# Performance work log

Hardware: AMD Instinct MI355X
Metric: run time of the kernel (lower is better)

Reference implementation:

```python
import jax, jax.numpy as jnp
import numpy as np
import math

B, T, C = 4, 2048, 1024
NH, D = 16, 64  # n_head, head_dim; NH * D == C


def setup_inputs() -> dict:
    key = jax.random.key(0)
    ks = jax.random.split(key, 7)
    std = 0.02
    return {
        "x": jax.random.normal(ks[0], (B, T, C), dtype=jnp.float32),
        "W_attn": jax.random.normal(ks[1], (C, 3 * C), dtype=jnp.float32) * std,
        "b_attn": jax.random.normal(ks[2], (3 * C,), dtype=jnp.float32) * std,
        "bQ": jax.random.normal(ks[3], (NH, D), dtype=jnp.float32) * 0.1 + 0.5,
        "bK": jax.random.normal(ks[4], (NH, D), dtype=jnp.float32) * 0.1 + 0.3,
        "W_proj": jax.random.normal(ks[5], (C, C), dtype=jnp.float32) * std,
        "b_proj": jax.random.normal(ks[6], (C,), dtype=jnp.float32) * std,
    }


def reference(x, W_attn, b_attn, bQ, bK, W_proj, b_proj):
    Bx, Tx, Cx = x.shape
    qkv = x @ W_attn + b_attn                      # [B, T, 3C]
    q, k, v = jnp.split(qkv, 3, axis=2)
    # [B, T, C] -> [B, NH, T, D]
    q = q.reshape(Bx, Tx, NH, D).transpose(0, 2, 1, 3)
    k = k.reshape(Bx, Tx, NH, D).transpose(0, 2, 1, 3)
    v = v.reshape(Bx, Tx, NH, D).transpose(0, 2, 1, 3)
    # per-head disorder bias added to Q and K before the dot product
    q = q + bQ[None, :, None, :]
    k = k + bK[None, :, None, :]
    scores = jnp.einsum('bhqd,bhkd->bhqk', q, k) / math.sqrt(D)  # [B, NH, T, T]
    causal = jnp.tril(jnp.ones((Tx, Tx), dtype=bool))
    scores = jnp.where(causal[None, None], scores, jnp.float32(-jnp.inf))
    att = jax.nn.softmax(scores, axis=-1)
    y = jnp.einsum('bhqk,bhkd->bhqd', att, v)      # [B, NH, T, D]
    y = y.transpose(0, 2, 1, 3).reshape(Bx, Tx, Cx)
    return y @ W_proj + b_proj
```

## Files before the change

### kernel.cpp

```cpp
#include <hip/hip_runtime.h>

typedef unsigned short u16;
typedef unsigned int u32;
typedef unsigned long long u64;
typedef __bf16 bf16x8 __attribute__((ext_vector_type(8)));
typedef float f32x4 __attribute__((ext_vector_type(4)));

#define B_  4
#define T_  2048
#define C_  1024
#define NH_ 16
#define D_  64
#define M_  (B_*T_)
#define N_QKV (3*C_)

#define ATTN_BLOCKS 1024

#define BARRIER()  __asm__ __volatile__("s_barrier" ::: "memory")
#define WAIT_VM4() __asm__ __volatile__("s_waitcnt vmcnt(4)" ::: "memory")
#define WAIT_VM8() __asm__ __volatile__("s_waitcnt vmcnt(8)" ::: "memory")
#define WAIT_VM0() __asm__ __volatile__("s_waitcnt vmcnt(0)" ::: "memory")
#define LGKM0()    __asm__ __volatile__("s_waitcnt lgkmcnt(0)" ::: "memory")

__device__ __forceinline__ void async_copy16(void* lds, const void* gptr) {
  __builtin_amdgcn_global_load_lds(
      (const __attribute__((address_space(1))) u32*)gptr,
      (__attribute__((address_space(3))) u32*)(u32)(uintptr_t)lds,
      16, 0, 0);
}

__device__ __forceinline__ u16 f2bf(float f) {
  union { float f; unsigned u; } c; c.f = f;
  unsigned u = c.u;
  unsigned r = (u + 0x7fffu + ((u >> 16) & 1u)) >> 16;
  return (u16)r;
}

__global__ __launch_bounds__(256) void conv_bf16(const float* __restrict__ in,
                                                 u16* __restrict__ out, int n) {
  int i = (blockIdx.x * 256 + threadIdx.x) * 4;
  if (i < n) {
    float4 f = *reinterpret_cast<const float4*>(in + i);
    u16 o[4] = { f2bf(f.x), f2bf(f.y), f2bf(f.z), f2bf(f.w) };
    *reinterpret_cast<uint2*>(out + i) = *reinterpret_cast<uint2*>(o);
  }
}

__global__ __launch_bounds__(256) void transpose_bf16(const float* __restrict__ in,
                                                      u16* __restrict__ out,
                                                      int K, int N) {
  __shared__ float tile[32][33];
  int bi = blockIdx.y;
  int bj = blockIdx.x;
  int tx = threadIdx.x & 31;
  int ty = threadIdx.x >> 5;
#pragma unroll
  for (int i = 0; i < 4; ++i) {
    int row = ty + i * 8;
    tile[row][tx] = in[(bi * 32 + row) * N + bj * 32 + tx];
  }
  __syncthreads();
#pragma unroll
  for (int i = 0; i < 4; ++i) {
    int row = ty + i * 8;
    out[(bj * 32 + row) * K + bi * 32 + tx] = f2bf(tile[tx][row]);
  }
}

__global__ __launch_bounds__(256, 2) void gemm_qkv(const u16* __restrict__ A,
                                                   const u16* __restrict__ Bt,
                                                   const float* __restrict__ b_attn,
                                                   const float* __restrict__ bQ,
                                                   const float* __restrict__ bK,
                                                   u16* __restrict__ qo,
                                                   u16* __restrict__ ko,
                                                   u16* __restrict__ vo) {
  const int K = C_;
  int bid = blockIdx.x;
  int wg = (bid & 7) * 192 + (bid >> 3);
  int bm = wg / 24, bn = wg % 24;
  const bool qk = (bn < 16);

  int tid = threadIdx.x;
  int wid = tid >> 6, lane = tid & 63;
  int lm = lane & 15, lq = lane >> 4;
  int wm = (wid >> 1) * 64, wn = (wid & 1) * 64;

  __shared__ u16 As[2][128 * 64];
  __shared__ u16 Bs[2][128 * 64];

  f32x4 acc[4][4];
#pragma unroll
  for (int i = 0; i < 4; ++i)
#pragma unroll
    for (int j = 0; j < 4; ++j) acc[i][j] = (f32x4){0.f, 0.f, 0.f, 0.f};

  const u16* Ab = A + (size_t)(bm * 128) * K;
  const u16* Bb = Bt + (size_t)(bn * 128) * K;
  int srow = lane >> 3;
  int sgc  = ((lane & 7) ^ srow) * 8;

  auto stage = [&](int bb, int t) {
#pragma unroll
    for (int i = 0; i < 4; ++i) {
      int c = i * 4 + wid;
      async_copy16(&As[bb][c * 512], Ab + (size_t)(c * 8 + srow) * K + t * 64 + sgc);
      async_copy16(&Bs[bb][c * 512], Bb + (size_t)(c * 8 + srow) * K + t * 64 + sgc);
    }
  };

  stage(0, 0);
  const int NT = K / 64;
  for (int t = 0; t < NT; ++t) {
    int bb = t & 1;
    int tn = (t + 1 < NT) ? t + 1 : t;
    stage(bb ^ 1, tn);
    WAIT_VM8();
    BARRIER();
    bf16x8 af[4][2], bf[4][2];
#pragma unroll
    for (int mt = 0; mt < 4; ++mt) {
      const u16* base = &As[bb][(wm + mt * 16 + lm) * 64];
#pragma unroll
      for (int kh = 0; kh < 2; ++kh)
        af[mt][kh] = *reinterpret_cast<const bf16x8*>(base + (((kh * 4 + lq) ^ (lm & 7)) * 8));
    }
#pragma unroll
    for (int nt = 0; nt < 4; ++nt) {
      const u16* base = &Bs[bb][(wn + nt * 16 + lm) * 64];
#pragma unroll
      for (int kh = 0; kh < 2; ++kh)
        bf[nt][kh] = *reinterpret_cast<const bf16x8*>(base + (((kh * 4 + lq) ^ (lm & 7)) * 8));
    }
    if (qk) {
#pragma unroll
      for (int mt = 0; mt < 4; ++mt)
#pragma unroll
        for (int nt = 0; nt < 4; ++nt)
#pragma unroll
          for (int kh = 0; kh < 2; ++kh)
            acc[mt][nt] = __builtin_amdgcn_mfma_f32_16x16x32_bf16(bf[nt][kh], af[mt][kh],
                                                                  acc[mt][nt], 0, 0, 0);
    } else {
#pragma unroll
      for (int mt = 0; mt < 4; ++mt)
#pragma unroll
        for (int nt = 0; nt < 4; ++nt)
#pragma unroll
          for (int kh = 0; kh < 2; ++kh)
            acc[mt][nt] = __builtin_amdgcn_mfma_f32_16x16x32_bf16(af[mt][kh], bf[nt][kh],
                                                                  acc[mt][nt], 0, 0, 0);
    }
    LGKM0();
    BARRIER();
  }
  WAIT_VM0();

  const float qscale = 0.18033688011112042f;
  if (qk) {
    const float* bvec = (bn < 8) ? bQ : bK;
    u16* outp = (bn < 8) ? qo : ko;
    float scale = (bn < 8) ? qscale : 1.0f;
#pragma unroll
    for (int mt = 0; mt < 4; ++mt) {
#pragma unroll
      for (int nt = 0; nt < 4; ++nt) {
        int n0 = bn * 128 + wn + nt * 16 + lq * 4;
        int m  = bm * 128 + wm + mt * 16 + lm;
        int c0 = n0 & 1023;
        int h = c0 >> 6;
        int d0 = c0 & 63;
        int b = m >> 11;
        int tt = m & 2047;
        float4 ba = *reinterpret_cast<const float4*>(&b_attn[n0]);
        float4 bb = *reinterpret_cast<const float4*>(&bvec[c0]);
        u16 wb[4];
        wb[0] = f2bf((acc[mt][nt][0] + ba.x + bb.x) * scale);
        wb[1] = f2bf((acc[mt][nt][1] + ba.y + bb.y) * scale);
        wb[2] = f2bf((acc[mt][nt][2] + ba.z + bb.z) * scale);
        wb[3] = f2bf((acc[mt][nt][3] + ba.w + bb.w) * scale);
        *reinterpret_cast<uint2*>(&outp[((size_t)(b * NH_ + h) * T_ + tt) * D_ + d0]) =
            *reinterpret_cast<uint2*>(wb);
      }
    }
  } else {
#pragma unroll
    for (int mt = 0; mt < 4; ++mt) {
#pragma unroll
      for (int nt = 0; nt < 4; ++nt) {
        int m0 = bm * 128 + wm + mt * 16 + lq * 4;
        int n = bn * 128 + wn + nt * 16 + lm;
        int c = n & 1023;
        int h = c >> 6;
        int d = c & 63;
        int b = m0 >> 11;
        int t0 = m0 & 2047;
        float bias = b_attn[n];
        u16 wb[4];
#pragma unroll
        for (int r = 0; r < 4; ++r) wb[r] = f2bf(acc[mt][nt][r] + bias);
        *reinterpret_cast<uint2*>(&vo[((size_t)(b * NH_ + h) * D_ + d) * T_ + t0]) =
            *reinterpret_cast<uint2*>(wb);
      }
    }
  }
}

__global__ __launch_bounds__(256, 4) void attn_kernel(const u16* __restrict__ q,
                                                      const u16* __restrict__ k,
                                                      const u16* __restrict__ vt,
                                                      u16* __restrict__ y) {
  int tid = threadIdx.x;
  int w = tid >> 6, lane = tid & 63;
  int lm = lane & 15, lq = lane >> 4;

  __shared__ u16 Ks[2][64 * 64];
  __shared__ u16 Vs[2][64 * 64];

  int srow = lane >> 3;
  int sg   = (lane & 7) ^ srow;

  int idx = blockIdx.x;
  int c8 = idx & 255, jq = idx >> 8;
  int a = c8 & 7, gq = c8 >> 3;
  int qt, bh;
  if (jq == 0)      { qt = 15 - a; bh = gq; }
  else if (jq == 1) { qt = 8 + a;  bh = 32 + gq; }
  else if (jq == 2) { qt = 7 - a;  bh = gq; }
  else              { qt = a;      bh = 32 + gq; }

  int b = bh >> 4, h = bh & 15;
  const int klast = 2 * qt + 1;
  const int qrow0 = qt * 128 + w * 32;

  const u16* qb = q + ((size_t)bh * T_ + qrow0) * D_;
  const u16* kb = k + (size_t)bh * T_ * D_;
  const u16* vb = vt + (size_t)bh * D_ * T_;

  auto stage_K = [&](int buf, int kbi) {
    const u16* gb = kb + (size_t)(kbi * 64) * 64;
#pragma unroll
    for (int j = 0; j < 2; ++j) {
      int c = w * 2 + j;
      async_copy16(&Ks[buf][c * 512], gb + (c * 8 + srow) * 64 + sg * 8);
    }
  };
  auto stage_V = [&](int buf, int kbi) {
    const u16* gb = vb + kbi * 64;
#pragma unroll
    for (int j = 0; j < 2; ++j) {
      int c = w * 2 + j;
      async_copy16(&Vs[buf][c * 512], gb + (size_t)(c * 8 + srow) * T_ + sg * 8);
    }
  };

  bf16x8 bq[2][2];
#pragma unroll
  for (int qt2 = 0; qt2 < 2; ++qt2) {
    const u16* qp = qb + (qt2 * 16 + lm) * D_ + lq * 8;
    bq[qt2][0] = *reinterpret_cast<const bf16x8*>(qp);
    bq[qt2][1] = *reinterpret_cast<const bf16x8*>(qp + 32);
  }

  f32x4 o[4][2];
#pragma unroll
  for (int dt = 0; dt < 4; ++dt)
#pragma unroll
    for (int qt2 = 0; qt2 < 2; ++qt2) o[dt][qt2] = (f32x4){0.f, 0.f, 0.f, 0.f};
  float mprev[2] = {-1e30f, -1e30f}, lsum[2] = {0.f, 0.f};

  stage_K(0, 0); stage_V(0, 0);
  stage_K(1, 1); stage_V(1, 1);

  for (int kbi = 0; kbi <= klast; ++kbi) {
    int buf = kbi & 1;
    WAIT_VM4();
    BARRIER();

    bf16x8 kf[4][2];
#pragma unroll
    for (int kt = 0; kt < 4; ++kt) {
      const u16* base = &Ks[buf][(kt * 16 + lm) * 64];
      kf[kt][0] = *reinterpret_cast<const bf16x8*>(base + ((lq ^ (lm & 7)) * 8));
      kf[kt][1] = *reinterpret_cast<const bf16x8*>(base + (((4 + lq) ^ (lm & 7)) * 8));
    }

    f32x4 s[4][2];
#pragma unroll
    for (int kt = 0; kt < 4; ++kt)
#pragma unroll
      for (int qt2 = 0; qt2 < 2; ++qt2) {
        f32x4 z = (f32x4){0.f, 0.f, 0.f, 0.f};
        z = __builtin_amdgcn_mfma_f32_16x16x32_bf16(kf[kt][0], bq[qt2][0], z, 0, 0, 0);
        z = __builtin_amdgcn_mfma_f32_16x16x32_bf16(kf[kt][1], bq[qt2][1], z, 0, 0, 0);
        s[kt][qt2] = z;
      }

    bool maskt = (kbi * 64 + 63 > qrow0);
    bf16x8 pb[2][2];
#pragma unroll
    for (int qt2 = 0; qt2 < 2; ++qt2) {
      int qg = qrow0 + qt2 * 16 + lm;
      if (maskt) {
#pragma unroll
        for (int kt = 0; kt < 4; ++kt)
#pragma unroll
          for (int r = 0; r < 4; ++r) {
            int key = kbi * 64 + kt * 16 + lq * 4 + r;
            if (key > qg) s[kt][qt2][r] = -1e30f;
          }
      }
      float mx[4];
#pragma unroll
      for (int kt = 0; kt < 4; ++kt)
        mx[kt] = fmaxf(fmaxf(s[kt][qt2][0], s[kt][qt2][1]),
                       fmaxf(s[kt][qt2][2], s[kt][qt2][3]));
      float mval = fmaxf(fmaxf(mx[0], mx[1]), fmaxf(mx[2], mx[3]));
      mval = fmaxf(mval, __shfl_xor(mval, 16));
      mval = fmaxf(mval, __shfl_xor(mval, 32));
      float mold = mprev[qt2];
      float mnew = fmaxf(mold, mval);
      unsigned long long upd = __ballot(mval > mold);
      if (upd) {
        float alpha = __builtin_exp2f(mold - mnew);
        lsum[qt2] *= alpha;
#pragma unroll
        for (int dt = 0; dt < 4; ++dt) o[dt][qt2] *= alpha;
        mprev[qt2] = mnew;
      }
      float rs = 0.f;
      unsigned pw[8];
#pragma unroll
      for (int kt = 0; kt < 4; ++kt) {
        unsigned pu[4];
#pragma unroll
        for (int r = 0; r < 4; ++r) {
          float p = __builtin_exp2f(s[kt][qt2][r] - mnew);
          rs += p;
          union { float f; unsigned u; } cc; cc.f = p;
          pu[r] = cc.u;
        }
        pw[kt * 2]     = __builtin_amdgcn_perm(pu[1], pu[0], 0x07060302u);
        pw[kt * 2 + 1] = __builtin_amdgcn_perm(pu[3], pu[2], 0x07060302u);
      }
      rs += __shfl_xor(rs, 16);
      rs += __shfl_xor(rs, 32);
      lsum[qt2] += rs;
      union { unsigned u[4]; bf16x8 v; } b0, b1;
#pragma unroll
      for (int t = 0; t < 4; ++t) { b0.u[t] = pw[t]; b1.u[t] = pw[4 + t]; }
      pb[qt2][0] = b0.v;
      pb[qt2][1] = b1.v;
    }

    {
      int r7 = lm & 7;
      int h4 = (lq & 1) * 4;
      int g0 = lq >> 1;
#pragma unroll
      for (int dt = 0; dt < 4; ++dt) {
        const u16* vbase = &Vs[buf][(dt * 16 + lm) * 64];
        union { u64 qd[2]; bf16x8 v; } t0, t1;
        t0.qd[0] = *reinterpret_cast<const u64*>(vbase + ((g0 ^ r7) * 8) + h4);
        t0.qd[1] = *reinterpret_cast<const u64*>(vbase + (((g0 + 2) ^ r7) * 8) + h4);
        t1.qd[0] = *reinterpret_cast<const u64*>(vbase + (((g0 + 4) ^ r7) * 8) + h4);
        t1.qd[1] = *reinterpret_cast<const u64*>(vbase + (((g0 + 6) ^ r7) * 8) + h4);
#pragma unroll
        for (int qt2 = 0; qt2 < 2; ++qt2) {
          o[dt][qt2] = __builtin_amdgcn_mfma_f32_16x16x32_bf16(t0.v, pb[qt2][0], o[dt][qt2], 0, 0, 0);
          o[dt][qt2] = __builtin_amdgcn_mfma_f32_16x16x32_bf16(t1.v, pb[qt2][1], o[dt][qt2], 0, 0, 0);
        }
      }
    }

    BARRIER();
    int nk = (kbi + 2 <= klast) ? kbi + 2 : klast;
    stage_K(buf, nk); stage_V(buf, nk);
  }

  WAIT_VM0();

#pragma unroll
  for (int qt2 = 0; qt2 < 2; ++qt2) {
    float inv = 1.f / lsum[qt2];
    int qg = qrow0 + qt2 * 16 + lm;
#pragma unroll
    for (int dt = 0; dt < 4; ++dt) {
      u16 wb[4];
#pragma unroll
      for (int r = 0; r < 4; ++r) wb[r] = f2bf(o[dt][qt2][r] * inv);
      int d = dt * 16 + lq * 4;
      *reinterpret_cast<uint2*>(&y[((size_t)(b * T_ + qg) * NH_ + h) * D_ + d]) =
          *reinterpret_cast<uint2*>(wb);
    }
  }
}

__global__ __launch_bounds__(256, 2) void gemm_proj(const u16* __restrict__ A,
                                                    const u16* __restrict__ Bt,
                                                    const float* __restrict__ b_proj,
                                                    float* __restrict__ out) {
  const int K = C_, N = C_;
  int bid = blockIdx.x;
  int wg = (bid & 7) * 64 + (bid >> 3);
  int bm = wg / 8, bn = wg % 8;

  int tid = threadIdx.x;
  int wid = tid >> 6, lane = tid & 63;
  int lm = lane & 15, lq = lane >> 4;
  int wm = (wid >> 1) * 64, wn = (wid & 1) * 64;

  __shared__ u16 As[2][128 * 64];
  __shared__ u16 Bs[2][128 * 64];

  f32x4 acc[4][4];
#pragma unroll
  for (int i = 0; i < 4; ++i)
#pragma unroll
    for (int j = 0; j < 4; ++j) acc[i][j] = (f32x4){0.f, 0.f, 0.f, 0.f};

  const u16* Ab = A + (size_t)(bm * 128) * K;
  const u16* Bb = Bt + (size_t)(bn * 128) * K;
  int srow = lane >> 3;
  int sgc  = ((lane & 7) ^ srow) * 8;

  auto stage = [&](int bb, int t) {
#pragma unroll
    for (int i = 0; i < 4; ++i) {
      int c = i * 4 + wid;
      async_copy16(&As[bb][c * 512], Ab + (size_t)(c * 8 + srow) * K + t * 64 + sgc);
      async_copy16(&Bs[bb][c * 512], Bb + (size_t)(c * 8 + srow) * K + t * 64 + sgc);
    }
  };

  stage(0, 0);
  const int NT = K / 64;
  for (int t = 0; t < NT; ++t) {
    int bb = t & 1;
    int tn = (t + 1 < NT) ? t + 1 : t;
    stage(bb ^ 1, tn);
    WAIT_VM8();
    BARRIER();
    bf16x8 af[4][2], bf[4][2];
#pragma unroll
    for (int mt = 0; mt < 4; ++mt) {
      const u16* base = &As[bb][(wm + mt * 16 + lm) * 64];
#pragma unroll
      for (int kh = 0; kh < 2; ++kh)
        af[mt][kh] = *reinterpret_cast<const bf16x8*>(base + (((kh * 4 + lq) ^ (lm & 7)) * 8));
    }
#pragma unroll
    for (int nt = 0; nt < 4; ++nt) {
      const u16* base = &Bs[bb][(wn + nt * 16 + lm) * 64];
#pragma unroll
      for (int kh = 0; kh < 2; ++kh)
        bf[nt][kh] = *reinterpret_cast<const bf16x8*>(base + (((kh * 4 + lq) ^ (lm & 7)) * 8));
    }
#pragma unroll
    for (int mt = 0; mt < 4; ++mt)
#pragma unroll
      for (int nt = 0; nt < 4; ++nt)
#pragma unroll
        for (int kh = 0; kh < 2; ++kh)
          acc[mt][nt] = __builtin_amdgcn_mfma_f32_16x16x32_bf16(af[mt][kh], bf[nt][kh],
                                                                acc[mt][nt], 0, 0, 0);
    LGKM0();
    BARRIER();
  }
  WAIT_VM0();

#pragma unroll
  for (int mt = 0; mt < 4; ++mt) {
#pragma unroll
    for (int nt = 0; nt < 4; ++nt) {
#pragma unroll
      for (int r = 0; r < 4; ++r) {
        int m = bm * 128 + wm + mt * 16 + lq * 4 + r;
        int n = bn * 128 + wn + nt * 16 + lm;
        out[(size_t)m * N + n] = acc[mt][nt][r] + b_proj[n];
      }
    }
  }
}

extern "C" void kernel_launch(void* const* d_in, const int* in_sizes, int n_in,
                              void* d_out, int out_size, void* d_ws, size_t ws_size,
                              hipStream_t stream) {
  const float* x      = (const float*)d_in[0];
  const float* W_attn = (const float*)d_in[1];
  const float* b_attn = (const float*)d_in[2];
  const float* bQ     = (const float*)d_in[3];
  const float* bK     = (const float*)d_in[4];
  const float* W_proj = (const float*)d_in[5];
  const float* b_proj = (const float*)d_in[6];
  float* out = (float*)d_out;

  char* ws = (char*)d_ws;
  u16* xb  = (u16*)(ws);
  u16* WaT = (u16*)(ws + 16777216);
  u16* WpT = (u16*)(ws + 23068672);
  u16* qw  = (u16*)(ws + 25165824);
  u16* kw  = (u16*)(ws + 41943040);
  u16* vw  = (u16*)(ws + 58720256);
  u16* yw  = (u16*)(ws + 75497472);

  conv_bf16<<<M_ * C_ / (4 * 256), 256, 0, stream>>>(x, xb, M_ * C_);
  {
    dim3 g(N_QKV / 32, C_ / 32);
    transpose_bf16<<<g, 256, 0, stream>>>(W_attn, WaT, C_, N_QKV);
  }
  {
    dim3 g(C_ / 32, C_ / 32);
    transpose_bf16<<<g, 256, 0, stream>>>(W_proj, WpT, C_, C_);
  }
  gemm_qkv<<<(M_ / 128) * (N_QKV / 128), 256, 0, stream>>>(xb, WaT, b_attn, bQ, bK, qw, kw, vw);
  attn_kernel<<<ATTN_BLOCKS, 256, 0, stream>>>(qw, kw, vw, yw);
  gemm_proj<<<(M_ / 128) * (C_ / 128), 256, 0, stream>>>(yw, WpT, b_proj, out);
}
```

Measured before the change: 285.9 us.

## Use lazy max rescaling, MFMA row sums, early V loads, vectorized proj stores

In the attention kernel, the running softmax max is now only updated when a new block max exceeds the old one by more than 8 (log2 units). This skips most rescale passes at the risk of larger unnormalised exponentials. The row sum is no longer built with shuffles; it comes from an extra MFMA of the probabilities against a ones vector, which also keeps the normaliser consistent with the bf16-rounded probabilities. V fragments are read from LDS before the softmax so their latency overlaps it. In the projection GEMM the MFMA operands are swapped so each lane holds four consecutive output columns, allowing float4 bias loads and stores instead of scalar strided writes.

```diff
diff --git a/kernel.cpp b/kernel.cpp
--- a/kernel.cpp
+++ b/kernel.cpp
@@ -262,12 +262,17 @@
     bq[qt2][1] = *reinterpret_cast<const bf16x8*>(qp + 32);
   }
 
-  f32x4 o[4][2];
+  const __bf16 one_ = (__bf16)1.0f;
+  const bf16x8 ones = (bf16x8){one_, one_, one_, one_, one_, one_, one_, one_};
+
+  f32x4 o[4][2], o5[2];
 #pragma unroll
   for (int dt = 0; dt < 4; ++dt)
 #pragma unroll
     for (int qt2 = 0; qt2 < 2; ++qt2) o[dt][qt2] = (f32x4){0.f, 0.f, 0.f, 0.f};
-  float mprev[2] = {-1e30f, -1e30f}, lsum[2] = {0.f, 0.f};
+  o5[0] = (f32x4){0.f, 0.f, 0.f, 0.f};
+  o5[1] = (f32x4){0.f, 0.f, 0.f, 0.f};
+  float mprev[2] = {-1e30f, -1e30f};
 
   stage_K(0, 0); stage_V(0, 0);
   stage_K(1, 1); stage_V(1, 1);
@@ -295,6 +300,24 @@
         z = __builtin_amdgcn_mfma_f32_16x16x32_bf16(kf[kt][1], bq[qt2][1], z, 0, 0, 0);
         s[kt][qt2] = z;
       }
+
+    bf16x8 vf[4][2];
+    {
+      int r7 = lm & 7;
+      int h4 = (lq & 1) * 4;
+      int g0 = lq >> 1;
+#pragma unroll
+      for (int dt = 0; dt < 4; ++dt) {
+        const u16* vbase = &Vs[buf][(dt * 16 + lm) * 64];
+        union { u64 qd[2]; bf16x8 v; } t0, t1;
+        t0.qd[0] = *reinterpret_cast<const u64*>(vbase + ((g0 ^ r7) * 8) + h4);
+        t0.qd[1] = *reinterpret_cast<const u64*>(vbase + (((g0 + 2) ^ r7) * 8) + h4);
+        t1.qd[0] = *reinterpret_cast<const u64*>(vbase + (((g0 + 4) ^ r7) * 8) + h4);
+        t1.qd[1] = *reinterpret_cast<const u64*>(vbase + (((g0 + 6) ^ r7) * 8) + h4);
+        vf[dt][0] = t0.v;
+        vf[dt][1] = t1.v;
+      }
+    }
 
     bool maskt = (kbi * 64 + 63 > qrow0);
     bf16x8 pb[2][2];
@@ -319,33 +342,28 @@
       mval = fmaxf(mval, __shfl_xor(mval, 16));
       mval = fmaxf(mval, __shfl_xor(mval, 32));
       float mold = mprev[qt2];
-      float mnew = fmaxf(mold, mval);
-      unsigned long long upd = __ballot(mval > mold);
-      if (upd) {
+      if (__ballot(mval > mold + 8.f)) {
+        float mnew = fmaxf(mold, mval);
         float alpha = __builtin_exp2f(mold - mnew);
-        lsum[qt2] *= alpha;
 #pragma unroll
         for (int dt = 0; dt < 4; ++dt) o[dt][qt2] *= alpha;
+        o5[qt2] *= alpha;
         mprev[qt2] = mnew;
       }
-      float rs = 0.f;
+      float m = mprev[qt2];
       unsigned pw[8];
 #pragma unroll
       for (int kt = 0; kt < 4; ++kt) {
         unsigned pu[4];
 #pragma unroll
         for (int r = 0; r < 4; ++r) {
-          float p = __builtin_exp2f(s[kt][qt2][r] - mnew);
-          rs += p;
+          float p = __builtin_exp2f(s[kt][qt2][r] - m);
           union { float f; unsigned u; } cc; cc.f = p;
           pu[r] = cc.u;
         }
         pw[kt * 2]     = __builtin_amdgcn_perm(pu[1], pu[0], 0x07060302u);
         pw[kt * 2 + 1] = __builtin_amdgcn_perm(pu[3], pu[2], 0x07060302u);
       }
-      rs += __shfl_xor(rs, 16);
-      rs += __shfl_xor(rs, 32);
-      lsum[qt2] += rs;
       union { unsigned u[4]; bf16x8 v; } b0, b1;
 #pragma unroll
       for (int t = 0; t < 4; ++t) { b0.u[t] = pw[t]; b1.u[t] = pw[4 + t]; }
@@ -353,24 +371,17 @@
       pb[qt2][1] = b1.v;
     }
 
-    {
-      int r7 = lm & 7;
-      int h4 = (lq & 1) * 4;
-      int g0 = lq >> 1;
-#pragma unroll
-      for (int dt = 0; dt < 4; ++dt) {
-        const u16* vbase = &Vs[buf][(dt * 16 + lm) * 64];
-        union { u64 qd[2]; bf16x8 v; } t0, t1;
-        t0.qd[0] = *reinterpret_cast<const u64*>(vbase + ((g0 ^ r7) * 8) + h4);
-        t0.qd[1] = *reinterpret_cast<const u64*>(vbase + (((g0 + 2) ^ r7) * 8) + h4);
-        t1.qd[0] = *reinterpret_cast<const u64*>(vbase + (((g0 + 4) ^ r7) * 8) + h4);
-        t1.qd[1] = *reinterpret_cast<const u64*>(vbase + (((g0 + 6) ^ r7) * 8) + h4);
-#pragma unroll
-        for (int qt2 = 0; qt2 < 2; ++qt2) {
-          o[dt][qt2] = __builtin_amdgcn_mfma_f32_16x16x32_bf16(t0.v, pb[qt2][0], o[dt][qt2], 0, 0, 0);
-          o[dt][qt2] = __builtin_amdgcn_mfma_f32_16x16x32_bf16(t1.v, pb[qt2][1], o[dt][qt2], 0, 0, 0);
-        }
-      }
+#pragma unroll
+    for (int dt = 0; dt < 4; ++dt)
+#pragma unroll
+      for (int qt2 = 0; qt2 < 2; ++qt2) {
+        o[dt][qt2] = __builtin_amdgcn_mfma_f32_16x16x32_bf16(vf[dt][0], pb[qt2][0], o[dt][qt2], 0, 0, 0);
+        o[dt][qt2] = __builtin_amdgcn_mfma_f32_16x16x32_bf16(vf[dt][1], pb[qt2][1], o[dt][qt2], 0, 0, 0);
+      }
+#pragma unroll
+    for (int qt2 = 0; qt2 < 2; ++qt2) {
+      o5[qt2] = __builtin_amdgcn_mfma_f32_16x16x32_bf16(ones, pb[qt2][0], o5[qt2], 0, 0, 0);
+      o5[qt2] = __builtin_amdgcn_mfma_f32_16x16x32_bf16(ones, pb[qt2][1], o5[qt2], 0, 0, 0);
     }
 
     BARRIER();
@@ -382,7 +393,7 @@
 
 #pragma unroll
   for (int qt2 = 0; qt2 < 2; ++qt2) {
-    float inv = 1.f / lsum[qt2];
+    float inv = 1.f / o5[qt2][0];
     int qg = qrow0 + qt2 * 16 + lm;
 #pragma unroll
     for (int dt = 0; dt < 4; ++dt) {
@@ -462,7 +473,7 @@
       for (int nt = 0; nt < 4; ++nt)
 #pragma unroll
         for (int kh = 0; kh < 2; ++kh)
-          acc[mt][nt] = __builtin_amdgcn_mfma_f32_16x16x32_bf16(af[mt][kh], bf[nt][kh],
+          acc[mt][nt] = __builtin_amdgcn_mfma_f32_16x16x32_bf16(bf[nt][kh], af[mt][kh],
                                                                 acc[mt][nt], 0, 0, 0);
     LGKM0();
     BARRIER();
@@ -473,12 +484,15 @@
   for (int mt = 0; mt < 4; ++mt) {
 #pragma unroll
     for (int nt = 0; nt < 4; ++nt) {
-#pragma unroll
-      for (int r = 0; r < 4; ++r) {
-        int m = bm * 128 + wm + mt * 16 + lq * 4 + r;
-        int n = bn * 128 + wn + nt * 16 + lm;
-        out[(size_t)m * N + n] = acc[mt][nt][r] + b_proj[n];
-      }
+      int n0 = bn * 128 + wn + nt * 16 + lq * 4;
+      int m  = bm * 128 + wm + mt * 16 + lm;
+      float4 bp = *reinterpret_cast<const float4*>(&b_proj[n0]);
+      float4 res;
+      res.x = acc[mt][nt][0] + bp.x;
+      res.y = acc[mt][nt][1] + bp.y;
+      res.z = acc[mt][nt][2] + bp.z;
+      res.w = acc[mt][nt][3] + bp.w;
+      *reinterpret_cast<float4*>(&out[(size_t)m * N + n0]) = res;
     }
   }
 }
```

New measurement: 396.3 us. +38.6%, slower.
